# Kernel optimization log

Hardware: AMD Instinct MI355X
Metric: run time of the kernel (lower is better)

Reference implementation:

```python
import jax, jax.numpy as jnp
import numpy as np

DIM = 1024
HDIM = 4 * DIM
E = 8        # num_routed_experts
TOP_K = 2
B, T = 2, 2048


def setup_inputs() -> dict:
    key = jax.random.key(0)
    ks = jax.random.split(key, 6)
    std = 0.5 * DIM ** -0.5  # matches original init scale
    return {
        "x": jax.random.normal(ks[0], (B, T, DIM), jnp.float32),
        "router_w": jax.random.normal(ks[1], (E, DIM), jnp.float32) * DIM ** -0.5,
        "w_shared_up": jax.random.uniform(ks[2], (DIM, HDIM), jnp.float32, -1.0, 1.0) * (3 ** 0.5 * std),
        "w_shared_down": jax.random.normal(ks[3], (DIM, HDIM), jnp.float32) * std,
        "w_routed_up": jax.random.uniform(ks[4], (E, DIM, HDIM), jnp.float32, -1.0, 1.0) * (3 ** 0.5 * std),
        "w_routed_down": jax.random.normal(ks[5], (E, DIM, HDIM), jnp.float32) * std,
    }


def reference(x, router_w, w_shared_up, w_shared_down, w_routed_up, w_routed_down):
    Bb, Tt, D = x.shape
    N = Bb * Tt
    xf = x.reshape(N, D)

    # --- routing ---
    logits = xf @ router_w.T                      # [N, E]
    probs = jax.nn.softmax(logits, axis=-1)
    topw, topi = jax.lax.top_k(probs, TOP_K)      # [N, K]
    topw = topw / jnp.sum(topw, axis=-1, keepdims=True)
    # per-token combine weights over experts (topk indices are distinct)
    comb = jnp.zeros((N, E), probs.dtype).at[jnp.arange(N)[:, None], topi].add(topw)

    # --- fused up projection: h_e = x @ W_shared_up + x @ W_routed_up[e] ---
    h_shared = xf @ w_shared_up                   # [N, H]
    h = h_shared[:, None, :] + jnp.einsum('nd,edh->neh', xf, w_routed_up)  # [N, E, H]
    h = jnp.square(jax.nn.relu(h))                # relu(h)^2

    # --- down projection: y_e = h_e @ W_shared_down.T + h_e @ W_routed_down[e].T ---
    y = jnp.einsum('neh,dh->ned', h, w_shared_down) \
        + jnp.einsum('neh,edh->ned', h, w_routed_down)  # [N, E, D]

    # --- combine (weighted scatter-add equivalent) ---
    out = jnp.einsum('ne,ned->nd', comb, y).reshape(Bb, Tt, D)

    # --- aux losses ---
    one_hot_top1 = jax.nn.one_hot(topi[:, 0], E, dtype=jnp.float32)
    tokens_per_expert = one_hot_top1.sum(axis=0)                 # [E]
    fraction_per_expert = tokens_per_expert / N
    avg_router_prob = probs.mean(axis=0)
    load_balancing_loss = E * jnp.sum(jax.lax.stop_gradient(fraction_per_expert) * avg_router_prob)
    router_z_loss = jnp.mean(jax.scipy.special.logsumexp(logits, axis=-1) ** 2)
    importance = probs.sum(axis=0)
    importance_loss = jnp.var(importance, ddof=1)  # torch.var is unbiased

    return (out, load_balancing_loss, router_z_loss, importance_loss, tokens_per_expert)
```

## Files before the change

kernel.cpp:

```cpp
#include <hip/hip_runtime.h>
#include <hip/hip_bf16.h>

#define N_TOK 4096
#define DIMD  1024
#define HDIM  4096
#define NEXP  8
#define MAXSLOT 9216
#define MAXTILE 72

typedef __attribute__((ext_vector_type(4))) float f32x4;
typedef __attribute__((ext_vector_type(8))) short bf16x8;

__device__ __forceinline__ ushort f2bf(float f) {
    __hip_bfloat16 h = __float2bfloat16(f);
    return *reinterpret_cast<ushort*>(&h);
}

__global__ __launch_bounds__(256) void router_kernel(
    const float* __restrict__ x, const float* __restrict__ rw,
    ushort* __restrict__ xbf, int* __restrict__ tok_e, float* __restrict__ tok_w,
    float* __restrict__ aux_f, int* __restrict__ aux_i)
{
    int wave = threadIdx.x >> 6, lane = threadIdx.x & 63;
    int token = blockIdx.x * 4 + wave;
    float acc[NEXP];
#pragma unroll
    for (int e = 0; e < NEXP; ++e) acc[e] = 0.f;
    const float* xr = x + (size_t)token * DIMD;
    for (int it = 0; it < DIMD / 64; ++it) {
        int d = it * 64 + lane;
        float xv = xr[d];
        xbf[(size_t)token * DIMD + d] = f2bf(xv);
#pragma unroll
        for (int e = 0; e < NEXP; ++e) acc[e] += xv * rw[e * DIMD + d];
    }
#pragma unroll
    for (int e = 0; e < NEXP; ++e) {
        float v = acc[e];
        for (int off = 32; off; off >>= 1) v += __shfl_xor(v, off);
        acc[e] = v;
    }
    float m = acc[0];
#pragma unroll
    for (int e = 1; e < NEXP; ++e) m = fmaxf(m, acc[e]);
    float p[NEXP], s = 0.f;
#pragma unroll
    for (int e = 0; e < NEXP; ++e) { p[e] = expf(acc[e] - m); s += p[e]; }
    float lse = m + logf(s);
    float inv = 1.f / s;
    int i1 = 0; float b1 = p[0];
#pragma unroll
    for (int e = 1; e < NEXP; ++e) if (p[e] > b1) { b1 = p[e]; i1 = e; }
    int i2 = -1; float b2 = -1.f;
#pragma unroll
    for (int e = 0; e < NEXP; ++e) if (e != i1 && p[e] > b2) { b2 = p[e]; i2 = e; }
    float wsum = b1 + b2;
    float w1 = b1 / wsum, w2 = b2 / wsum;
    if (lane == 0) {
        tok_e[token * 2] = i1; tok_e[token * 2 + 1] = i2;
        tok_w[token * 2] = w1; tok_w[token * 2 + 1] = w2;
    }
    __shared__ float s_imp[NEXP]; __shared__ float s_z;
    __shared__ int s_c1[NEXP], s_c2[NEXP];
    if (threadIdx.x < NEXP) { s_imp[threadIdx.x] = 0.f; s_c1[threadIdx.x] = 0; s_c2[threadIdx.x] = 0; }
    if (threadIdx.x == 0) s_z = 0.f;
    __syncthreads();
    if (lane == 0) {
#pragma unroll
        for (int e = 0; e < NEXP; ++e) atomicAdd(&s_imp[e], p[e] * inv);
        atomicAdd(&s_z, lse * lse);
        atomicAdd(&s_c1[i1], 1);
        atomicAdd(&s_c2[i1], 1);
        atomicAdd(&s_c2[i2], 1);
    }
    __syncthreads();
    if (threadIdx.x < NEXP) {
        atomicAdd(&aux_f[threadIdx.x], s_imp[threadIdx.x]);
        atomicAdd(&aux_i[threadIdx.x], s_c1[threadIdx.x]);
        atomicAdd(&aux_i[NEXP + threadIdx.x], s_c2[threadIdx.x]);
    }
    if (threadIdx.x == 0) atomicAdd(&aux_f[NEXP], s_z);
}

__global__ void finalize_kernel(const float* __restrict__ aux_f, const int* __restrict__ aux_i,
                                float* __restrict__ out_tail, int* __restrict__ offsets,
                                int* __restrict__ cursor, int* __restrict__ tile_e)
{
    if (threadIdx.x != 0 || blockIdx.x != 0) return;
    float imp[NEXP];
    float lb = 0.f, isum = 0.f;
    for (int e = 0; e < NEXP; ++e) {
        imp[e] = aux_f[e];
        isum += imp[e];
        lb += (float)aux_i[e] * imp[e];
    }
    lb *= (float)NEXP / ((float)N_TOK * (float)N_TOK);
    float zl = aux_f[NEXP] / (float)N_TOK;
    float mean = isum / (float)NEXP;
    float var = 0.f;
    for (int e = 0; e < NEXP; ++e) { float d = imp[e] - mean; var += d * d; }
    var /= (float)(NEXP - 1);
    out_tail[0] = lb;
    out_tail[1] = zl;
    out_tail[2] = var;
    for (int e = 0; e < NEXP; ++e) out_tail[3 + e] = (float)aux_i[e];

    int off = 0;
    for (int e = 0; e < NEXP; ++e) {
        offsets[e] = off;
        off += ((aux_i[NEXP + e] + 127) >> 7) << 7;
    }
    offsets[NEXP] = off;
    int ntile = off >> 7;
    for (int tt = 0; tt < MAXTILE; ++tt) {
        int e = -1;
        if (tt < ntile) {
            for (int j = 0; j < NEXP; ++j)
                if (tt * 128 >= offsets[j] && tt * 128 < offsets[j + 1]) e = j;
        }
        tile_e[tt] = e;
    }
    for (int e = 0; e < NEXP; ++e) cursor[e] = 0;
}

__global__ void fill_kernel(const int* __restrict__ tok_e, const float* __restrict__ tok_w,
                            const int* __restrict__ offsets, int* __restrict__ cursor,
                            int* __restrict__ slot_token, float* __restrict__ slot_wt)
{
    int t = blockIdx.x * 256 + threadIdx.x;
    if (t >= N_TOK) return;
    for (int k = 0; k < 2; ++k) {
        int e = tok_e[t * 2 + k];
        int pos = atomicAdd(&cursor[e], 1);
        int slot = offsets[e] + pos;
        slot_token[slot] = t;
        slot_wt[slot] = tok_w[t * 2 + k];
    }
}

__global__ __launch_bounds__(256) void convert_up(const float* __restrict__ wsu,
                                                  const float* __restrict__ wru,
                                                  ushort* __restrict__ wup)
{
    int e = blockIdx.z;
    int h0 = blockIdx.x * 64, d0 = blockIdx.y * 64;
    __shared__ float tile[64][65];
    int c = threadIdx.x & 63, r4 = threadIdx.x >> 6;
#pragma unroll
    for (int it = 0; it < 16; ++it) {
        int r = it * 4 + r4;
        size_t gi = ((size_t)(d0 + r)) * HDIM + h0 + c;
        tile[r][c] = wsu[gi] + wru[(size_t)e * DIMD * HDIM + gi];
    }
    __syncthreads();
#pragma unroll
    for (int it = 0; it < 16; ++it) {
        int hr = it * 4 + r4;
        float v = tile[c][hr];
        wup[((size_t)e * HDIM + h0 + hr) * DIMD + d0 + c] = f2bf(v);
    }
}

__global__ void convert_dn(const float* __restrict__ wsd, const float* __restrict__ wrd,
                           ushort* __restrict__ wdn)
{
    size_t i = ((size_t)blockIdx.x * 256 + threadIdx.x) * 4;
    float4 a = *(const float4*)(wrd + i);
    float4 b = *(const float4*)(wsd + (i & (size_t)0x3FFFFF));
    ushort4 o;
    o.x = f2bf(a.x + b.x); o.y = f2bf(a.y + b.y);
    o.z = f2bf(a.z + b.z); o.w = f2bf(a.w + b.w);
    *(ushort4*)(wdn + i) = o;
}

__global__ __launch_bounds__(256) void up_gemm(
    const ushort* __restrict__ xbf, const ushort* __restrict__ wup,
    const int* __restrict__ slot_token, const int* __restrict__ tile_e,
    ushort* __restrict__ hbf)
{
    int bt = blockIdx.y;
    int e = tile_e[bt];
    if (e < 0) return;
    int h0 = blockIdx.x * 128;
    __shared__ ushort As[128 * 72];
    __shared__ ushort Bs[128 * 72];
    __shared__ int stok[128];
    int t = threadIdx.x;
    if (t < 128) stok[t] = slot_token[bt * 128 + t];
    int wave = t >> 6, lane = t & 63;
    int wm = (wave >> 1) << 6, wn = (wave & 1) << 6;
    int l15 = lane & 15, q = lane >> 4;
    f32x4 acc[4][4] = {};
    const ushort* wb = wup + ((size_t)e * HDIM + h0) * DIMD;
    for (int k0 = 0; k0 < DIMD; k0 += 64) {
        __syncthreads();
#pragma unroll
        for (int it = 0; it < 4; ++it) {
            int seg = t + it * 256;
            int r = seg >> 3, part = seg & 7;
            int tok = stok[r];
            int4 v = {0, 0, 0, 0};
            if (tok >= 0) v = *(const int4*)(xbf + (size_t)tok * DIMD + k0 + part * 8);
            *(int4*)(As + r * 72 + part * 8) = v;
            int4 w = *(const int4*)(wb + (size_t)r * DIMD + k0 + part * 8);
            *(int4*)(Bs + r * 72 + part * 8) = w;
        }
        __syncthreads();
#pragma unroll
        for (int kk = 0; kk < 64; kk += 32) {
            int ko = kk + q * 8;
            bf16x8 a[4], b[4];
#pragma unroll
            for (int i = 0; i < 4; ++i) a[i] = *(const bf16x8*)(As + (wm + i * 16 + l15) * 72 + ko);
#pragma unroll
            for (int j = 0; j < 4; ++j) b[j] = *(const bf16x8*)(Bs + (wn + j * 16 + l15) * 72 + ko);
#pragma unroll
            for (int i = 0; i < 4; ++i)
#pragma unroll
                for (int j = 0; j < 4; ++j)
                    acc[i][j] = __builtin_amdgcn_mfma_f32_16x16x32_bf16(a[i], b[j], acc[i][j], 0, 0, 0);
        }
    }
    size_t rowbase = (size_t)bt * 128;
#pragma unroll
    for (int i = 0; i < 4; ++i) {
        int row = wm + i * 16 + q * 4;
#pragma unroll
        for (int r = 0; r < 4; ++r) {
            size_t rb = (rowbase + row + r) * HDIM + h0;
#pragma unroll
            for (int j = 0; j < 4; ++j) {
                float v = acc[i][j][r];
                v = fmaxf(v, 0.f); v = v * v;
                hbf[rb + wn + j * 16 + l15] = f2bf(v);
            }
        }
    }
}

__global__ __launch_bounds__(256) void down_gemm(
    const ushort* __restrict__ hbf, const ushort* __restrict__ wdn,
    const int* __restrict__ slot_token, const float* __restrict__ slot_wt,
    const int* __restrict__ tile_e, float* __restrict__ out)
{
    int bt = blockIdx.y;
    int e = tile_e[bt];
    if (e < 0) return;
    int d0 = blockIdx.x * 128;
    __shared__ ushort As[128 * 72];
    __shared__ ushort Bs[128 * 72];
    __shared__ int stok[128];
    __shared__ float swt[128];
    int t = threadIdx.x;
    if (t < 128) { stok[t] = slot_token[bt * 128 + t]; swt[t] = slot_wt[bt * 128 + t]; }
    int wave = t >> 6, lane = t & 63;
    int wm = (wave >> 1) << 6, wn = (wave & 1) << 6;
    int l15 = lane & 15, q = lane >> 4;
    f32x4 acc[4][4] = {};
    const ushort* ab = hbf + (size_t)bt * 128 * HDIM;
    const ushort* wb = wdn + ((size_t)e * DIMD + d0) * HDIM;
    for (int k0 = 0; k0 < HDIM; k0 += 64) {
        __syncthreads();
#pragma unroll
        for (int it = 0; it < 4; ++it) {
            int seg = t + it * 256;
            int r = seg >> 3, part = seg & 7;
            *(int4*)(As + r * 72 + part * 8) = *(const int4*)(ab + (size_t)r * HDIM + k0 + part * 8);
            *(int4*)(Bs + r * 72 + part * 8) = *(const int4*)(wb + (size_t)r * HDIM + k0 + part * 8);
        }
        __syncthreads();
#pragma unroll
        for (int kk = 0; kk < 64; kk += 32) {
            int ko = kk + q * 8;
            bf16x8 a[4], b[4];
#pragma unroll
            for (int i = 0; i < 4; ++i) a[i] = *(const bf16x8*)(As + (wm + i * 16 + l15) * 72 + ko);
#pragma unroll
            for (int j = 0; j < 4; ++j) b[j] = *(const bf16x8*)(Bs + (wn + j * 16 + l15) * 72 + ko);
#pragma unroll
            for (int i = 0; i < 4; ++i)
#pragma unroll
                for (int j = 0; j < 4; ++j)
                    acc[i][j] = __builtin_amdgcn_mfma_f32_16x16x32_bf16(a[i], b[j], acc[i][j], 0, 0, 0);
        }
    }
#pragma unroll
    for (int i = 0; i < 4; ++i) {
#pragma unroll
        for (int r = 0; r < 4; ++r) {
            int row = wm + i * 16 + q * 4 + r;
            int tok = stok[row];
            if (tok < 0) continue;
            float wgt = swt[row];
            float* orow = out + (size_t)tok * DIMD + d0 + wn;
#pragma unroll
            for (int j = 0; j < 4; ++j)
                atomicAdd(orow + j * 16 + l15, wgt * acc[i][j][r]);
        }
    }
}

extern "C" void kernel_launch(void* const* d_in, const int* in_sizes, int n_in,
                              void* d_out, int out_size, void* d_ws, size_t ws_size,
                              hipStream_t stream)
{
    const float* x   = (const float*)d_in[0];
    const float* rw  = (const float*)d_in[1];
    const float* wsu = (const float*)d_in[2];
    const float* wsd = (const float*)d_in[3];
    const float* wru = (const float*)d_in[4];
    const float* wrd = (const float*)d_in[5];
    float* out = (float*)d_out;

    char* ws = (char*)d_ws;
    size_t off = 0;
    auto alloc = [&](size_t b) { size_t o = off; off = (off + b + 255) & ~(size_t)255; return o; };
    float* aux_f     = (float*)(ws + alloc(16 * 4));
    int*   aux_i     = (int*)(ws + alloc(16 * 4));
    int*   tok_e     = (int*)(ws + alloc(N_TOK * 2 * 4));
    float* tok_w     = (float*)(ws + alloc(N_TOK * 2 * 4));
    int*   offsets   = (int*)(ws + alloc(16 * 4));
    int*   cursor    = (int*)(ws + alloc(8 * 4));
    int*   tile_e    = (int*)(ws + alloc(128 * 4));
    int*   slot_token= (int*)(ws + alloc(MAXSLOT * 4));
    float* slot_wt   = (float*)(ws + alloc(MAXSLOT * 4));
    ushort* xbf      = (ushort*)(ws + alloc((size_t)N_TOK * DIMD * 2));
    ushort* wup      = (ushort*)(ws + alloc((size_t)NEXP * HDIM * DIMD * 2));
    ushort* wdn      = (ushort*)(ws + alloc((size_t)NEXP * DIMD * HDIM * 2));
    ushort* hbf      = (ushort*)(ws + alloc((size_t)MAXSLOT * HDIM * 2));
    (void)ws_size; (void)in_sizes; (void)n_in;

    hipMemsetAsync(d_out, 0, (size_t)out_size * 4, stream);
    hipMemsetAsync(aux_f, 0, 16 * 4, stream);
    hipMemsetAsync(aux_i, 0, 16 * 4, stream);
    hipMemsetAsync(slot_token, 0xFF, MAXSLOT * 4, stream);

    router_kernel<<<N_TOK / 4, 256, 0, stream>>>(x, rw, xbf, tok_e, tok_w, aux_f, aux_i);
    finalize_kernel<<<1, 64, 0, stream>>>(aux_f, aux_i, out + (size_t)N_TOK * DIMD,
                                          offsets, cursor, tile_e);
    fill_kernel<<<N_TOK / 256, 256, 0, stream>>>(tok_e, tok_w, offsets, cursor, slot_token, slot_wt);
    convert_up<<<dim3(HDIM / 64, DIMD / 64, NEXP), 256, 0, stream>>>(wsu, wru, wup);
    convert_dn<<<(NEXP * DIMD * HDIM) / (256 * 4), 256, 0, stream>>>(wsd, wrd, wdn);
    up_gemm<<<dim3(HDIM / 128, MAXTILE), 256, 0, stream>>>(xbf, wup, slot_token, tile_e, hbf);
    down_gemm<<<dim3(DIMD / 128, MAXTILE), 256, 0, stream>>>(hbf, wdn, slot_token, slot_wt, tile_e, out);
}
```

Before: 810.2 us.

## Use direct global-to-LDS loads with XOR swizzle, split-K down GEMM, vectorize convert_up

Both grouped GEMMs now stage tiles through global_load_lds async copies into unpadded, XOR-swizzled LDS tiles instead of register round-trips into padded tiles. This is meant to cut VGPR traffic and LDS bank conflicts. The down GEMM is split in two along K (grid z=2) to double the block count, which relies on the epilogue accumulating into out atomically. convert_up's transposed write now emits 4-wide bf16 stores. Padded slots are clamped to token 0 rather than zero-filled, so their junk rows must stay masked in the down epilogue.

```diff
diff --git a/kernel.cpp b/kernel.cpp
--- a/kernel.cpp
+++ b/kernel.cpp
@@ -14,6 +14,12 @@
 __device__ __forceinline__ ushort f2bf(float f) {
     __hip_bfloat16 h = __float2bfloat16(f);
     return *reinterpret_cast<ushort*>(&h);
+}
+
+__device__ __forceinline__ void async_copy16(const ushort* g, ushort* l) {
+    __builtin_amdgcn_global_load_lds((const __attribute__((address_space(1))) void*)g,
+                                     (__attribute__((address_space(3))) void*)l,
+                                     16, 0, 0);
 }
 
 __global__ __launch_bounds__(256) void router_kernel(
@@ -153,11 +159,16 @@
         tile[r][c] = wsu[gi] + wru[(size_t)e * DIMD * HDIM + gi];
     }
     __syncthreads();
-#pragma unroll
-    for (int it = 0; it < 16; ++it) {
-        int hr = it * 4 + r4;
-        float v = tile[c][hr];
-        wup[((size_t)e * HDIM + h0 + hr) * DIMD + d0 + c] = f2bf(v);
+    int c4 = threadIdx.x & 15, rr = threadIdx.x >> 4;
+#pragma unroll
+    for (int it = 0; it < 4; ++it) {
+        int hr = it * 16 + rr;
+        ushort4 o;
+        o.x = f2bf(tile[c4 * 4 + 0][hr]);
+        o.y = f2bf(tile[c4 * 4 + 1][hr]);
+        o.z = f2bf(tile[c4 * 4 + 2][hr]);
+        o.w = f2bf(tile[c4 * 4 + 3][hr]);
+        *(ushort4*)(wup + ((size_t)e * HDIM + h0 + hr) * DIMD + d0 + c4 * 4) = o;
     }
 }
 
@@ -182,38 +193,46 @@
     int e = tile_e[bt];
     if (e < 0) return;
     int h0 = blockIdx.x * 128;
-    __shared__ ushort As[128 * 72];
-    __shared__ ushort Bs[128 * 72];
-    __shared__ int stok[128];
+    __shared__ ushort As[128 * 64];
+    __shared__ ushort Bs[128 * 64];
     int t = threadIdx.x;
-    if (t < 128) stok[t] = slot_token[bt * 128 + t];
     int wave = t >> 6, lane = t & 63;
+    int s8 = lane & 7, r8 = lane >> 3;
+    int p = s8 ^ r8;
+    const ushort* wb = wup + ((size_t)e * HDIM + h0) * DIMD;
+    const ushort* aptr[4];
+    const ushort* bptr[4];
+#pragma unroll
+    for (int cc = 0; cc < 4; ++cc) {
+        int row = wave * 32 + cc * 8 + r8;
+        int tok = slot_token[bt * 128 + row];
+        if (tok < 0) tok = 0;
+        aptr[cc] = xbf + (size_t)tok * DIMD + p * 8;
+        bptr[cc] = wb + (size_t)row * DIMD + p * 8;
+    }
+    ushort* lA = As + wave * 4 * 512;
+    ushort* lB = Bs + wave * 4 * 512;
     int wm = (wave >> 1) << 6, wn = (wave & 1) << 6;
     int l15 = lane & 15, q = lane >> 4;
+    int r7 = l15 & 7;
     f32x4 acc[4][4] = {};
-    const ushort* wb = wup + ((size_t)e * HDIM + h0) * DIMD;
     for (int k0 = 0; k0 < DIMD; k0 += 64) {
         __syncthreads();
 #pragma unroll
-        for (int it = 0; it < 4; ++it) {
-            int seg = t + it * 256;
-            int r = seg >> 3, part = seg & 7;
-            int tok = stok[r];
-            int4 v = {0, 0, 0, 0};
-            if (tok >= 0) v = *(const int4*)(xbf + (size_t)tok * DIMD + k0 + part * 8);
-            *(int4*)(As + r * 72 + part * 8) = v;
-            int4 w = *(const int4*)(wb + (size_t)r * DIMD + k0 + part * 8);
-            *(int4*)(Bs + r * 72 + part * 8) = w;
+        for (int cc = 0; cc < 4; ++cc) {
+            async_copy16(aptr[cc] + k0, lA + cc * 512);
+            async_copy16(bptr[cc] + k0, lB + cc * 512);
         }
         __syncthreads();
 #pragma unroll
         for (int kk = 0; kk < 64; kk += 32) {
-            int ko = kk + q * 8;
+            int pr = (kk >> 3) + q;
+            int so = ((pr ^ r7) << 3);
             bf16x8 a[4], b[4];
 #pragma unroll
-            for (int i = 0; i < 4; ++i) a[i] = *(const bf16x8*)(As + (wm + i * 16 + l15) * 72 + ko);
-#pragma unroll
-            for (int j = 0; j < 4; ++j) b[j] = *(const bf16x8*)(Bs + (wn + j * 16 + l15) * 72 + ko);
+            for (int i = 0; i < 4; ++i) a[i] = *(const bf16x8*)(As + (wm + i * 16 + l15) * 64 + so);
+#pragma unroll
+            for (int j = 0; j < 4; ++j) b[j] = *(const bf16x8*)(Bs + (wn + j * 16 + l15) * 64 + so);
 #pragma unroll
             for (int i = 0; i < 4; ++i)
 #pragma unroll
@@ -247,36 +266,47 @@
     int e = tile_e[bt];
     if (e < 0) return;
     int d0 = blockIdx.x * 128;
-    __shared__ ushort As[128 * 72];
-    __shared__ ushort Bs[128 * 72];
+    int kbase = blockIdx.z * (HDIM / 2);
+    __shared__ ushort As[128 * 64];
+    __shared__ ushort Bs[128 * 64];
     __shared__ int stok[128];
     __shared__ float swt[128];
     int t = threadIdx.x;
     if (t < 128) { stok[t] = slot_token[bt * 128 + t]; swt[t] = slot_wt[bt * 128 + t]; }
     int wave = t >> 6, lane = t & 63;
+    int s8 = lane & 7, r8 = lane >> 3;
+    int p = s8 ^ r8;
+    const ushort* aptr[4];
+    const ushort* bptr[4];
+#pragma unroll
+    for (int cc = 0; cc < 4; ++cc) {
+        int row = wave * 32 + cc * 8 + r8;
+        aptr[cc] = hbf + ((size_t)bt * 128 + row) * HDIM + p * 8;
+        bptr[cc] = wdn + ((size_t)e * DIMD + d0 + row) * HDIM + p * 8;
+    }
+    ushort* lA = As + wave * 4 * 512;
+    ushort* lB = Bs + wave * 4 * 512;
     int wm = (wave >> 1) << 6, wn = (wave & 1) << 6;
     int l15 = lane & 15, q = lane >> 4;
+    int r7 = l15 & 7;
     f32x4 acc[4][4] = {};
-    const ushort* ab = hbf + (size_t)bt * 128 * HDIM;
-    const ushort* wb = wdn + ((size_t)e * DIMD + d0) * HDIM;
-    for (int k0 = 0; k0 < HDIM; k0 += 64) {
+    for (int k0 = kbase; k0 < kbase + HDIM / 2; k0 += 64) {
         __syncthreads();
 #pragma unroll
-        for (int it = 0; it < 4; ++it) {
-            int seg = t + it * 256;
-            int r = seg >> 3, part = seg & 7;
-            *(int4*)(As + r * 72 + part * 8) = *(const int4*)(ab + (size_t)r * HDIM + k0 + part * 8);
-            *(int4*)(Bs + r * 72 + part * 8) = *(const int4*)(wb + (size_t)r * HDIM + k0 + part * 8);
+        for (int cc = 0; cc < 4; ++cc) {
+            async_copy16(aptr[cc] + k0, lA + cc * 512);
+            async_copy16(bptr[cc] + k0, lB + cc * 512);
         }
         __syncthreads();
 #pragma unroll
         for (int kk = 0; kk < 64; kk += 32) {
-            int ko = kk + q * 8;
+            int pr = (kk >> 3) + q;
+            int so = ((pr ^ r7) << 3);
             bf16x8 a[4], b[4];
 #pragma unroll
-            for (int i = 0; i < 4; ++i) a[i] = *(const bf16x8*)(As + (wm + i * 16 + l15) * 72 + ko);
-#pragma unroll
-            for (int j = 0; j < 4; ++j) b[j] = *(const bf16x8*)(Bs + (wn + j * 16 + l15) * 72 + ko);
+            for (int i = 0; i < 4; ++i) a[i] = *(const bf16x8*)(As + (wm + i * 16 + l15) * 64 + so);
+#pragma unroll
+            for (int j = 0; j < 4; ++j) b[j] = *(const bf16x8*)(Bs + (wn + j * 16 + l15) * 64 + so);
 #pragma unroll
             for (int i = 0; i < 4; ++i)
 #pragma unroll
@@ -342,5 +372,5 @@
     convert_up<<<dim3(HDIM / 64, DIMD / 64, NEXP), 256, 0, stream>>>(wsu, wru, wup);
     convert_dn<<<(NEXP * DIMD * HDIM) / (256 * 4), 256, 0, stream>>>(wsd, wrd, wdn);
     up_gemm<<<dim3(HDIM / 128, MAXTILE), 256, 0, stream>>>(xbf, wup, slot_token, tile_e, hbf);
-    down_gemm<<<dim3(DIMD / 128, MAXTILE), 256, 0, stream>>>(hbf, wdn, slot_token, slot_wt, tile_e, out);
-}
+    down_gemm<<<dim3(DIMD / 128, MAXTILE, 2), 256, 0, stream>>>(hbf, wdn, slot_token, slot_wt, tile_e, out);
+}
```

Result: faster. 697.5 us (-13.9%).
